# Kernel optimization log

Measured on AMD Instinct MI355X. Metric: run time of the kernel, lower is better.

## Reference

```python
import jax, jax.numpy as jnp
import numpy as np

INPUT_DIM = 128
HIDDEN_DIM = 128
NUM_NODE = 1_000_000

def setup_inputs() -> dict:
    key = jax.random.key(0)
    k_adj, k_emb, k_w, k_b = jax.random.split(key, 4)
    B, S, T, K = 16, 32, 32, 16
    adj_org = jax.random.randint(k_adj, (B, S, T, K), 0, NUM_NODE + 1, dtype=jnp.int32)
    # Embedding table (num_node+1, input_dim); row 0 zeroed as in reset_parameters
    emb = jax.random.normal(k_emb, (NUM_NODE + 1, INPUT_DIM), dtype=jnp.float32) * 0.05
    emb = emb.at[0].set(0.0)
    # NeighborAggregator weight and SageGCN self weight b
    W = jax.random.normal(k_w, (INPUT_DIM, HIDDEN_DIM), dtype=jnp.float32) * (1.0 / np.sqrt(INPUT_DIM))
    b = jax.random.normal(k_b, (INPUT_DIM, HIDDEN_DIM), dtype=jnp.float32) * (1.0 / np.sqrt(INPUT_DIM))
    return {"adj_org": adj_org, "emb": emb, "W": W, "b": b}

def reference(adj_org, emb, W, b):
    # Gather node features: [B,S,T,K,D]
    x = emb[adj_org]
    x_self = x[:, :, :, 0, :]          # [B,S,T,D]
    x_nei = x[:, :, :, 1:, :]          # [B,S,T,K-1,D]
    # mean neighbor aggregation (aggr_method='mean', aggr_hidden_method='sum')
    agg = x_nei.mean(axis=3)           # [B,S,T,D]
    neighbor_hidden = jnp.einsum('bstd,dh->bsth', agg, W)
    self_hidden = jnp.einsum('bstd,dh->bsth', x_self, b)
    hidden = jax.nn.relu(self_hidden + neighbor_hidden)  # SageGCN activation
    # GraphSage forward applies an extra relu after each layer (idempotent here)
    return jax.nn.relu(hidden)
```

## Files before the change

kernel.cpp:

```cpp
#include <hip/hip_runtime.h>
#include <hip/hip_bf16.h>


constexpr int DIM   = 128;
constexpr int KN    = 16;
constexpr int RPB   = 16;
constexpr int NROWS = 16 * 32 * 32;
constexpr int LDA   = 264;

typedef __bf16 bf16x8 __attribute__((ext_vector_type(8)));
typedef float  f32x4  __attribute__((ext_vector_type(4)));

__device__ __forceinline__ unsigned short f2b(float x) {
    __bf16 h = (__bf16)x;
    return __builtin_bit_cast(unsigned short, h);
}

__global__ __launch_bounds__(256, 4)
void graphsage_mfma(const int* __restrict__ adj,
                    const float* __restrict__ emb,
                    const float* __restrict__ W,
                    const float* __restrict__ Bm,
                    float* __restrict__ out)
{
    __shared__ unsigned short ldsA[RPB * LDA];
    __shared__ int idx_lds[RPB * KN];

    const int t    = threadIdx.x;
    const int row0 = blockIdx.x * RPB;

    idx_lds[t] = adj[row0 * KN + t];
    __syncthreads();

    {
        const int r     = t >> 4;
        const int c16   = t & 15;
        const int dbase = c16 * 8;
        float4 x0, x1;
        float4 a0 = make_float4(0.f, 0.f, 0.f, 0.f);
        float4 a1 = make_float4(0.f, 0.f, 0.f, 0.f);
        #pragma unroll
        for (int k = 0; k < KN; ++k) {
            const int e = idx_lds[r * KN + k];
            const float4* p =
                reinterpret_cast<const float4*>(emb + (size_t)e * DIM + dbase);
            const float4 v0 = p[0];
            const float4 v1 = p[1];
            if (k == 0) { x0 = v0; x1 = v1; }
            else {
                a0.x += v0.x; a0.y += v0.y; a0.z += v0.z; a0.w += v0.w;
                a1.x += v1.x; a1.y += v1.y; a1.z += v1.z; a1.w += v1.w;
            }
        }
        const float s = 1.0f / 15.0f;
        union { unsigned short u[8]; uint4 q; } pa, px;
        pa.u[0] = f2b(a0.x * s); pa.u[1] = f2b(a0.y * s);
        pa.u[2] = f2b(a0.z * s); pa.u[3] = f2b(a0.w * s);
        pa.u[4] = f2b(a1.x * s); pa.u[5] = f2b(a1.y * s);
        pa.u[6] = f2b(a1.z * s); pa.u[7] = f2b(a1.w * s);
        px.u[0] = f2b(x0.x); px.u[1] = f2b(x0.y);
        px.u[2] = f2b(x0.z); px.u[3] = f2b(x0.w);
        px.u[4] = f2b(x1.x); px.u[5] = f2b(x1.y);
        px.u[6] = f2b(x1.z); px.u[7] = f2b(x1.w);
        *reinterpret_cast<uint4*>(&ldsA[r * LDA + c16 * 8])        = pa.q;
        *reinterpret_cast<uint4*>(&ldsA[r * LDA + (16 + c16) * 8]) = px.q;
    }
    __syncthreads();

    {
        const int wid  = t >> 6;
        const int lane = t & 63;
        const int col  = lane & 15;
        const int g    = lane >> 4;
        const int n0   = wid * 32;

        f32x4 acc0 = {0.f, 0.f, 0.f, 0.f};
        f32x4 acc1 = {0.f, 0.f, 0.f, 0.f};
        const int arow = lane & 15;

        #pragma unroll
        for (int s = 0; s < 8; ++s) {
            const int c = s * 4 + g;
            bf16x8 a = __builtin_bit_cast(bf16x8,
                *reinterpret_cast<const uint4*>(&ldsA[arow * LDA + c * 8]));
            const float* __restrict__ M = (s < 4) ? W : Bm;
            const int k0 = (s & 3) * 32 + g * 8;
            union { unsigned short u[8]; bf16x8 v; } b0u, b1u;
            #pragma unroll
            for (int j = 0; j < 8; ++j) {
                const float* rowp = M + (size_t)(k0 + j) * DIM + n0;
                b0u.u[j] = f2b(rowp[col]);
                b1u.u[j] = f2b(rowp[16 + col]);
            }
            acc0 = __builtin_amdgcn_mfma_f32_16x16x32_bf16(a, b0u.v, acc0, 0, 0, 0);
            acc1 = __builtin_amdgcn_mfma_f32_16x16x32_bf16(a, b1u.v, acc1, 0, 0, 0);
        }

        #pragma unroll
        for (int reg = 0; reg < 4; ++reg) {
            const int rr = g * 4 + reg;
            float* o = out + (size_t)(row0 + rr) * DIM;
            o[n0 + col]      = fmaxf(acc0[reg], 0.0f);
            o[n0 + 16 + col] = fmaxf(acc1[reg], 0.0f);
        }
    }
}

extern "C" void kernel_launch(void* const* d_in, const int* in_sizes, int n_in,
                              void* d_out, int out_size, void* d_ws, size_t ws_size,
                              hipStream_t stream) {
    const int*   adj = (const int*)  d_in[0];
    const float* emb = (const float*)d_in[1];
    const float* W   = (const float*)d_in[2];
    const float* b   = (const float*)d_in[3];
    float*       out = (float*)d_out;

    graphsage_mfma<<<dim3(NROWS / RPB), dim3(256), 0, stream>>>(adj, emb, W, b, out);
}
```

Before: 28.24 us.

## Double block size to split neighbor gather and MFMA columns across more threads

```diff
diff --git a/kernel.cpp b/kernel.cpp
--- a/kernel.cpp
+++ b/kernel.cpp
@@ -16,7 +16,7 @@
     return __builtin_bit_cast(unsigned short, h);
 }
 
-__global__ __launch_bounds__(256, 4)
+__global__ __launch_bounds__(512, 4)
 void graphsage_mfma(const int* __restrict__ adj,
                     const float* __restrict__ emb,
                     const float* __restrict__ W,
@@ -29,41 +29,49 @@
     const int t    = threadIdx.x;
     const int row0 = blockIdx.x * RPB;
 
-    idx_lds[t] = adj[row0 * KN + t];
+    if (t < RPB * KN) idx_lds[t] = adj[row0 * KN + t];
     __syncthreads();
 
     {
-        const int r     = t >> 4;
+        const int r     = t >> 5;
         const int c16   = t & 15;
+        const int half  = (t >> 4) & 1;
         const int dbase = c16 * 8;
-        float4 x0, x1;
-        float4 a0 = make_float4(0.f, 0.f, 0.f, 0.f);
-        float4 a1 = make_float4(0.f, 0.f, 0.f, 0.f);
+        float4 x0 = make_float4(0.f,0.f,0.f,0.f), x1 = make_float4(0.f,0.f,0.f,0.f);
+        float4 a0 = make_float4(0.f,0.f,0.f,0.f), a1 = make_float4(0.f,0.f,0.f,0.f);
         #pragma unroll
-        for (int k = 0; k < KN; ++k) {
-            const int e = idx_lds[r * KN + k];
+        for (int k = 0; k < 8; ++k) {
+            const int kk = half * 8 + k;
+            const int e  = idx_lds[r * KN + kk];
             const float4* p =
                 reinterpret_cast<const float4*>(emb + (size_t)e * DIM + dbase);
             const float4 v0 = p[0];
             const float4 v1 = p[1];
-            if (k == 0) { x0 = v0; x1 = v1; }
+            if (half == 0 && k == 0) { x0 = v0; x1 = v1; }
             else {
                 a0.x += v0.x; a0.y += v0.y; a0.z += v0.z; a0.w += v0.w;
                 a1.x += v1.x; a1.y += v1.y; a1.z += v1.z; a1.w += v1.w;
             }
         }
-        const float s = 1.0f / 15.0f;
-        union { unsigned short u[8]; uint4 q; } pa, px;
-        pa.u[0] = f2b(a0.x * s); pa.u[1] = f2b(a0.y * s);
-        pa.u[2] = f2b(a0.z * s); pa.u[3] = f2b(a0.w * s);
-        pa.u[4] = f2b(a1.x * s); pa.u[5] = f2b(a1.y * s);
-        pa.u[6] = f2b(a1.z * s); pa.u[7] = f2b(a1.w * s);
-        px.u[0] = f2b(x0.x); px.u[1] = f2b(x0.y);
-        px.u[2] = f2b(x0.z); px.u[3] = f2b(x0.w);
-        px.u[4] = f2b(x1.x); px.u[5] = f2b(x1.y);
-        px.u[6] = f2b(x1.z); px.u[7] = f2b(x1.w);
-        *reinterpret_cast<uint4*>(&ldsA[r * LDA + c16 * 8])        = pa.q;
-        *reinterpret_cast<uint4*>(&ldsA[r * LDA + (16 + c16) * 8]) = px.q;
+        #pragma unroll
+        for (int j = 0; j < 4; ++j) {
+            (&a0.x)[j] += __shfl_xor((&a0.x)[j], 16, 64);
+            (&a1.x)[j] += __shfl_xor((&a1.x)[j], 16, 64);
+        }
+        if (half == 0) {
+            const float s = 1.0f / 15.0f;
+            union { unsigned short u[8]; uint4 q; } pa, px;
+            pa.u[0] = f2b(a0.x * s); pa.u[1] = f2b(a0.y * s);
+            pa.u[2] = f2b(a0.z * s); pa.u[3] = f2b(a0.w * s);
+            pa.u[4] = f2b(a1.x * s); pa.u[5] = f2b(a1.y * s);
+            pa.u[6] = f2b(a1.z * s); pa.u[7] = f2b(a1.w * s);
+            px.u[0] = f2b(x0.x); px.u[1] = f2b(x0.y);
+            px.u[2] = f2b(x0.z); px.u[3] = f2b(x0.w);
+            px.u[4] = f2b(x1.x); px.u[5] = f2b(x1.y);
+            px.u[6] = f2b(x1.z); px.u[7] = f2b(x1.w);
+            *reinterpret_cast<uint4*>(&ldsA[r * LDA + c16 * 8])        = pa.q;
+            *reinterpret_cast<uint4*>(&ldsA[r * LDA + (16 + c16) * 8]) = px.q;
+        }
     }
     __syncthreads();
 
@@ -72,10 +80,9 @@
         const int lane = t & 63;
         const int col  = lane & 15;
         const int g    = lane >> 4;
-        const int n0   = wid * 32;
+        const int n0   = wid * 16;
 
-        f32x4 acc0 = {0.f, 0.f, 0.f, 0.f};
-        f32x4 acc1 = {0.f, 0.f, 0.f, 0.f};
+        f32x4 acc = {0.f, 0.f, 0.f, 0.f};
         const int arow = lane & 15;
 
         #pragma unroll
@@ -85,23 +92,18 @@
                 *reinterpret_cast<const uint4*>(&ldsA[arow * LDA + c * 8]));
             const float* __restrict__ M = (s < 4) ? W : Bm;
             const int k0 = (s & 3) * 32 + g * 8;
-            union { unsigned short u[8]; bf16x8 v; } b0u, b1u;
+            union { unsigned short u[8]; bf16x8 v; } bu;
             #pragma unroll
             for (int j = 0; j < 8; ++j) {
-                const float* rowp = M + (size_t)(k0 + j) * DIM + n0;
-                b0u.u[j] = f2b(rowp[col]);
-                b1u.u[j] = f2b(rowp[16 + col]);
+                bu.u[j] = f2b(M[(size_t)(k0 + j) * DIM + n0 + col]);
             }
-            acc0 = __builtin_amdgcn_mfma_f32_16x16x32_bf16(a, b0u.v, acc0, 0, 0, 0);
-            acc1 = __builtin_amdgcn_mfma_f32_16x16x32_bf16(a, b1u.v, acc1, 0, 0, 0);
+            acc = __builtin_amdgcn_mfma_f32_16x16x32_bf16(a, bu.v, acc, 0, 0, 0);
         }
 
         #pragma unroll
         for (int reg = 0; reg < 4; ++reg) {
             const int rr = g * 4 + reg;
-            float* o = out + (size_t)(row0 + rr) * DIM;
-            o[n0 + col]      = fmaxf(acc0[reg], 0.0f);
-            o[n0 + 16 + col] = fmaxf(acc1[reg], 0.0f);
+            out[(size_t)(row0 + rr) * DIM + n0 + col] = fmaxf(acc[reg], 0.0f);
         }
     }
 }
@@ -115,5 +117,5 @@
     const float* b   = (const float*)d_in[3];
     float*       out = (float*)d_out;
 
-    graphsage_mfma<<<dim3(NROWS / RPB), dim3(256), 0, stream>>>(adj, emb, W, b, out);
+    graphsage_mfma<<<dim3(NROWS / RPB), dim3(512), 0, stream>>>(adj, emb, W, b, out);
 }
```

After: 30.69 us. +8.7%, slower.
